# Kernel tuning notes

Measured on AMD Instinct MI355X. Metric: run time of the kernel, lower is better.

The kernel has to match this reference:

```python
import jax, jax.numpy as jnp
import numpy as np

SEQ_LEN = 252; WIN = 96; LEADS = 12; SECONDS = 10
LAYERS = 12; HEADS = 8; E = 128; FF = 512; B = 128
S = SEQ_LEN + LEADS  # 264 tokens after cls_token concat


def setup_inputs() -> dict:
    key = jax.random.key(0)
    ks = jax.random.split(key, 16)
    def n(k, shape, s=0.02):
        return jax.random.normal(k, shape, jnp.float32) * s
    return {
        "x": jax.random.normal(ks[0], (B, SEQ_LEN, WIN), jnp.float32),
        "t_indices": jax.random.randint(ks[1], (B, SEQ_LEN), 0, SECONDS + 1),
        "spatial_indices": jax.random.randint(ks[2], (B, SEQ_LEN), 0, LEADS + 1),
        "conv_w": n(ks[3], (E, WIN)),          # Conv1d k=1 == linear over window dim
        "conv_b": n(ks[4], (E,)),
        "pos_embed": n(ks[5], (1, S, E)),
        "time_tab": n(ks[6], (SECONDS + 1, E)),  # stacked time_embed_set
        "spat_tab": n(ks[7], (LEADS + 1, E)),    # stacked sqatial_embed_set
        "cls_token": n(ks[8], (1, LEADS, E)),
        "Wqkv": n(ks[9], (LAYERS, 3 * E, E)), "bqkv": jnp.zeros((LAYERS, 3 * E)),
        "Wo": n(ks[10], (LAYERS, E, E)), "bo": jnp.zeros((LAYERS, E)),
        "W1": n(ks[11], (LAYERS, FF, E)), "b1": jnp.zeros((LAYERS, FF)),
        "W2": n(ks[12], (LAYERS, E, FF)), "b2": jnp.zeros((LAYERS, E)),
        "ln1_g": jnp.ones((LAYERS, E)), "ln1_b": jnp.zeros((LAYERS, E)),
        "ln2_g": jnp.ones((LAYERS, E)), "ln2_b": jnp.zeros((LAYERS, E)),
    }


def _ln(x, g, b, eps=1e-5):
    m = x.mean(-1, keepdims=True)
    v = ((x - m) ** 2).mean(-1, keepdims=True)
    return (x - m) * jax.lax.rsqrt(v + eps) * g + b


def reference(x, t_indices, spatial_indices, conv_w, conv_b, pos_embed,
              time_tab, spat_tab, cls_token, Wqkv, bqkv, Wo, bo,
              W1, b1, W2, b2, ln1_g, ln1_b, ln2_g, ln2_b):
    Bn = x.shape[0]
    D = E // HEADS
    # kernel-size-1 Conv1d over window channels == per-token linear
    h = jnp.einsum('blt,et->ble', x, conv_w) + conv_b        # [B, L, E]
    h = jnp.concatenate([jnp.broadcast_to(cls_token, (Bn, LEADS, E)), h], axis=1)
    h = h + pos_embed                                        # [B, S, E]
    # vectorized replacement of the B*L python-loop gather
    h = h.at[:, LEADS:, :].add(time_tab[t_indices] + spat_tab[spatial_indices])
    # dropout: eval mode (identity)
    for i in range(LAYERS):  # post-norm TransformerEncoderLayer, relu FFN
        qkv = h @ Wqkv[i].T + bqkv[i]
        q, k, v = jnp.split(qkv, 3, axis=-1)
        q = q.reshape(Bn, S, HEADS, D)
        k = k.reshape(Bn, S, HEADS, D)
        v = v.reshape(Bn, S, HEADS, D)
        att = jax.nn.softmax(jnp.einsum('bqhd,bkhd->bhqk', q, k) / np.sqrt(D).astype(np.float32), axis=-1)
        o = jnp.einsum('bhqk,bkhd->bqhd', att, v).reshape(Bn, S, E) @ Wo[i].T + bo[i]
        h = _ln(h + o, ln1_g[i], ln1_b[i])
        ff = jax.nn.relu(h @ W1[i].T + b1[i]) @ W2[i].T + b2[i]
        h = _ln(h + ff, ln2_g[i], ln2_b[i])
    return h
```

## Files before the change

kernel.cpp:

```cpp
#include <hip/hip_runtime.h>

typedef unsigned short u16;
typedef __attribute__((ext_vector_type(8))) short s16x8;
typedef __attribute__((ext_vector_type(4))) float f32x4;

__device__ __forceinline__ float bf2f(u16 u) {
    union { unsigned i; float f; } v; v.i = (unsigned)u << 16; return v.f;
}
__device__ __forceinline__ u16 f2bf(float f) {
    union { float f; unsigned i; } v; v.f = f;
    unsigned r = v.i + 0x7fffu + ((v.i >> 16) & 1u);
    return (u16)(r >> 16);
}
__device__ __forceinline__ f32x4 mfma16(s16x8 a, s16x8 b, f32x4 c) {
    return __builtin_amdgcn_mfma_f32_16x16x32_bf16(a, b, c, 0, 0, 0);
}

__global__ __launch_bounds__(256)
void cvt_kernel(const float* __restrict__ src, u16* __restrict__ dst, int n)
{
    for (int i = blockIdx.x * 256 + threadIdx.x; i < n; i += gridDim.x * 256)
        dst[i] = f2bf(src[i]);
}

__global__ __launch_bounds__(256)
void embed_cls_kernel(const float* __restrict__ cls, const float* __restrict__ pos,
                      float* __restrict__ h32, u16* __restrict__ h16)
{
    int i = blockIdx.x * 256 + threadIdx.x;
    int e = i & 127, s = (i >> 7) % 12, b = i / (12 * 128);
    float v = cls[s * 128 + e] + pos[s * 128 + e];
    size_t o = ((size_t)b * 264 + s) * 128 + e;
    h32[o] = v; h16[o] = f2bf(v);
}

__global__ __launch_bounds__(256)
void embed_mfma(const u16* __restrict__ x16, const u16* __restrict__ cw16,
                const float* __restrict__ cb, const float* __restrict__ pos,
                const float* __restrict__ ttab, const float* __restrict__ stab,
                const int* __restrict__ tidx, const int* __restrict__ sidx,
                float* __restrict__ h32, u16* __restrict__ h16)
{
    const int t = threadIdx.x;
    const int wave = t >> 6, lane = t & 63;
    const int quad = lane >> 4, l16 = lane & 15;
    const int n0 = wave * 32;

    s16x8 wf[2][3];
    float bv[2];
    #pragma unroll
    for (int nt = 0; nt < 2; ++nt) {
        bv[nt] = cb[n0 + nt * 16 + l16];
        #pragma unroll
        for (int ks = 0; ks < 3; ++ks)
            wf[nt][ks] = *(const s16x8*)&cw16[(n0 + nt * 16 + l16) * 96 + ks * 32 + quad * 8];
    }
    #pragma unroll
    for (int tt = 0; tt < 4; ++tt) {
        const int m0 = (blockIdx.x * 4 + tt) * 16;
        s16x8 af[3];
        #pragma unroll
        for (int ks = 0; ks < 3; ++ks)
            af[ks] = *(const s16x8*)&x16[(size_t)(m0 + l16) * 96 + ks * 32 + quad * 8];
        f32x4 a0 = (f32x4){0.f,0.f,0.f,0.f}, a1 = (f32x4){0.f,0.f,0.f,0.f};
        #pragma unroll
        for (int ks = 0; ks < 3; ++ks) {
            a0 = mfma16(af[ks], wf[0][ks], a0);
            a1 = mfma16(af[ks], wf[1][ks], a1);
        }
        #pragma unroll
        for (int r = 0; r < 4; ++r) {
            int row = m0 + quad * 4 + r;
            int b = row / 252, l = row - b * 252;
            int ti = tidx[row], si = sidx[row];
            size_t tok = (size_t)b * 264 + 12 + l;
            #pragma unroll
            for (int nt = 0; nt < 2; ++nt) {
                int col = n0 + nt * 16 + l16;
                float v = (nt ? a1[r] : a0[r]) + bv[nt]
                        + pos[(12 + l) * 128 + col]
                        + ttab[ti * 128 + col] + stab[si * 128 + col];
                h32[tok * 128 + col] = v;
                h16[tok * 128 + col] = f2bf(v);
            }
        }
    }
}

template<bool RELU>
__global__ __launch_bounds__(256)
void gemm_bias(const u16* __restrict__ A, const u16* __restrict__ W,
               const float* __restrict__ bias, u16* __restrict__ C,
               int N, int K)
{
    const int LDK = 136;
    __shared__ alignas(16) u16 As[64 * 136];
    __shared__ alignas(16) u16 Ws[64 * 136];
    const int m0 = blockIdx.x * 64;
    const int n0 = blockIdx.y * 64;
    const int t = threadIdx.x;
    const int wave = t >> 6, lane = t & 63;
    const int quad = lane >> 4, l16 = lane & 15;
    const int wm = (wave & 1) * 32, wn = (wave >> 1) * 32;

    f32x4 acc[2][2];
    #pragma unroll
    for (int i = 0; i < 2; ++i)
        #pragma unroll
        for (int j = 0; j < 2; ++j) acc[i][j] = (f32x4){0.f, 0.f, 0.f, 0.f};

    for (int kc = 0; kc < K; kc += 128) {
        __syncthreads();
        #pragma unroll
        for (int i = 0; i < 4; ++i) {
            int id = i * 256 + t;
            int row = id >> 4, c8 = (id & 15) << 3;
            *(uint4*)&As[row * LDK + c8] = *(const uint4*)&A[(size_t)(m0 + row) * K + kc + c8];
            *(uint4*)&Ws[row * LDK + c8] = *(const uint4*)&W[(size_t)(n0 + row) * K + kc + c8];
        }
        __syncthreads();
        #pragma unroll
        for (int ks = 0; ks < 4; ++ks) {
            s16x8 a0 = *(const s16x8*)&As[(wm + l16) * LDK + ks * 32 + quad * 8];
            s16x8 a1 = *(const s16x8*)&As[(wm + 16 + l16) * LDK + ks * 32 + quad * 8];
            s16x8 b0 = *(const s16x8*)&Ws[(wn + l16) * LDK + ks * 32 + quad * 8];
            s16x8 b1 = *(const s16x8*)&Ws[(wn + 16 + l16) * LDK + ks * 32 + quad * 8];
            acc[0][0] = mfma16(a0, b0, acc[0][0]);
            acc[0][1] = mfma16(a0, b1, acc[0][1]);
            acc[1][0] = mfma16(a1, b0, acc[1][0]);
            acc[1][1] = mfma16(a1, b1, acc[1][1]);
        }
    }
    #pragma unroll
    for (int ni = 0; ni < 2; ++ni) {
        int col = n0 + wn + ni * 16 + l16;
        float bv = bias[col];
        #pragma unroll
        for (int mi = 0; mi < 2; ++mi) {
            #pragma unroll
            for (int r = 0; r < 4; ++r) {
                int row = m0 + wm + mi * 16 + quad * 4 + r;
                float v = acc[mi][ni][r] + bv;
                if (RELU) v = fmaxf(v, 0.f);
                C[(size_t)row * N + col] = f2bf(v);
            }
        }
    }
}

template<int K>
__global__ __launch_bounds__(256)
void gemm_ln(const u16* __restrict__ A, const u16* __restrict__ W,
             const float* __restrict__ bias, const float* resid,
             const float* __restrict__ g, const float* __restrict__ be,
             float* o32, u16* o16)
{
    const int LDK = 136;
    __shared__ alignas(16) u16 As[64 * 136];
    __shared__ alignas(16) u16 Ws[128 * 136];
    const int m0 = blockIdx.x * 64;
    const int t = threadIdx.x;
    const int wave = t >> 6, lane = t & 63;
    const int quad = lane >> 4, l16 = lane & 15;
    const int wr = wave * 16;

    f32x4 acc[8];
    #pragma unroll
    for (int i = 0; i < 8; ++i) acc[i] = (f32x4){0.f, 0.f, 0.f, 0.f};

    for (int kc = 0; kc < K; kc += 128) {
        __syncthreads();
        #pragma unroll
        for (int i = 0; i < 4; ++i) {
            int id = i * 256 + t;
            int row = id >> 4, c8 = (id & 15) << 3;
            *(uint4*)&As[row * LDK + c8] = *(const uint4*)&A[(size_t)(m0 + row) * K + kc + c8];
        }
        #pragma unroll
        for (int i = 0; i < 8; ++i) {
            int id = i * 256 + t;
            int row = id >> 4, c8 = (id & 15) << 3;
            *(uint4*)&Ws[row * LDK + c8] = *(const uint4*)&W[(size_t)row * K + kc + c8];
        }
        __syncthreads();
        #pragma unroll
        for (int ks = 0; ks < 4; ++ks) {
            s16x8 a = *(const s16x8*)&As[(wr + l16) * LDK + ks * 32 + quad * 8];
            #pragma unroll
            for (int nt = 0; nt < 8; ++nt) {
                s16x8 b = *(const s16x8*)&Ws[(nt * 16 + l16) * LDK + ks * 32 + quad * 8];
                acc[nt] = mfma16(a, b, acc[nt]);
            }
        }
    }
    #pragma unroll
    for (int nt = 0; nt < 8; ++nt) {
        int col = nt * 16 + l16;
        float bv = bias[col];
        #pragma unroll
        for (int r = 0; r < 4; ++r) {
            int row = m0 + wr + quad * 4 + r;
            acc[nt][r] += bv + resid[(size_t)row * 128 + col];
        }
    }
    float sm[4], sq[4];
    #pragma unroll
    for (int r = 0; r < 4; ++r) {
        float s = 0.f, q = 0.f;
        #pragma unroll
        for (int nt = 0; nt < 8; ++nt) { float v = acc[nt][r]; s += v; q += v * v; }
        sm[r] = s; sq[r] = q;
    }
    #pragma unroll
    for (int mk = 1; mk < 16; mk <<= 1) {
        #pragma unroll
        for (int r = 0; r < 4; ++r) {
            sm[r] += __shfl_xor(sm[r], mk, 64);
            sq[r] += __shfl_xor(sq[r], mk, 64);
        }
    }
    #pragma unroll
    for (int r = 0; r < 4; ++r) {
        float mean = sm[r] * (1.f / 128.f);
        float var = sq[r] * (1.f / 128.f) - mean * mean;
        float rstd = rsqrtf(var + 1e-5f);
        int row = m0 + wr + quad * 4 + r;
        #pragma unroll
        for (int nt = 0; nt < 8; ++nt) {
            int col = nt * 16 + l16;
            float y = (acc[nt][r] - mean) * rstd * g[col] + be[col];
            o32[(size_t)row * 128 + col] = y;
            o16[(size_t)row * 128 + col] = f2bf(y);
        }
    }
}

__global__ __launch_bounds__(256)
void attn_kernel(const u16* __restrict__ qkv, u16* __restrict__ ctx)
{
    const int STR = 296;
    const int KLD = 24;
    __shared__ alignas(16) u16 VT[16 * STR];
    __shared__ alignas(16) u16 Ks[272 * KLD];
    const int b = blockIdx.x >> 3, h = blockIdx.x & 7;
    const size_t base = (size_t)b * 264 * 384;
    const int t = threadIdx.x;
    const int wave = t >> 6, lane = t & 63;
    const int quad = lane >> 4, l16 = lane & 15;
    const int hq = h * 16;

    for (int i = t; i < 264 * 2; i += 256) {
        int key = i >> 1, dq = (i & 1) * 8;
        *(uint4*)&Ks[key * KLD + dq] =
            *(const uint4*)&qkv[base + (size_t)key * 384 + 128 + hq + dq];
    }
    for (int i = t; i < 264 * 16; i += 256) {
        int s = i >> 4, d = i & 15;
        VT[d * STR + s] = qkv[base + (size_t)s * 384 + 256 + hq + d];
    }
    for (int i = t; i < 16 * 32; i += 256) {
        int d = i >> 5, c = 264 + (i & 31);
        VT[d * STR + c] = 0;
    }
    __syncthreads();

    for (int qt = wave; qt < 17; qt += 4) {
        const int q0 = qt * 16;
        s16x8 qf = (s16x8){0, 0, 0, 0, 0, 0, 0, 0};
        {
            int qrow = q0 + l16;
            if (quad < 2 && qrow < 264)
                qf = *(const s16x8*)&qkv[base + (size_t)qrow * 384 + hq + quad * 8];
        }
        f32x4 sc[17];
        #pragma unroll
        for (int kt = 0; kt < 17; ++kt) {
            s16x8 kf = (s16x8){0, 0, 0, 0, 0, 0, 0, 0};
            if (quad < 2)
                kf = *(const s16x8*)&Ks[(kt * 16 + l16) * KLD + quad * 8];
            f32x4 z = (f32x4){0.f, 0.f, 0.f, 0.f};
            sc[kt] = mfma16(kf, qf, z);
        }
        float mx = -1e30f;
        #pragma unroll
        for (int kt = 0; kt < 17; ++kt) {
            #pragma unroll
            for (int r = 0; r < 4; ++r) {
                float s = sc[kt][r] * 0.25f;
                if (kt == 16 && quad >= 2) s = -1e30f;
                sc[kt][r] = s;
                mx = fmaxf(mx, s);
            }
        }
        mx = fmaxf(mx, __shfl_xor(mx, 16, 64));
        mx = fmaxf(mx, __shfl_xor(mx, 32, 64));
        float ls = 0.f;
        #pragma unroll
        for (int kt = 0; kt < 17; ++kt) {
            #pragma unroll
            for (int r = 0; r < 4; ++r) {
                float e = __expf(sc[kt][r] - mx);
                sc[kt][r] = e;
                ls += e;
            }
        }
        ls += __shfl_xor(ls, 16, 64);
        ls += __shfl_xor(ls, 32, 64);
        float rinv = 1.f / ls;

        f32x4 oa = (f32x4){0.f, 0.f, 0.f, 0.f};
        #pragma unroll
        for (int c = 0; c < 9; ++c) {
            const int kt0 = 2 * c, kt1 = 2 * c + 1;
            union { s16x8 v; u16 u[8]; } pk;
            #pragma unroll
            for (int j = 0; j < 4; ++j) pk.u[j] = f2bf(sc[kt0][j] * rinv);
            #pragma unroll
            for (int j = 0; j < 4; ++j)
                pk.u[4 + j] = (c == 8) ? (u16)0 : f2bf(sc[kt1][j] * rinv);
            union { s16x8 v; uint2 h2[2]; } vt;
            vt.h2[0] = *(const uint2*)&VT[l16 * STR + kt0 * 16 + quad * 4];
            vt.h2[1] = *(const uint2*)&VT[l16 * STR + kt1 * 16 + quad * 4];
            oa = mfma16(pk.v, vt.v, oa);
        }
        #pragma unroll
        for (int r = 0; r < 4; ++r) {
            int row = q0 + quad * 4 + r;
            if (row < 264)
                ctx[((size_t)b * 264 + row) * 128 + hq + l16] = f2bf(oa[r]);
        }
    }
}

extern "C" void kernel_launch(void* const* d_in, const int* in_sizes, int n_in,
                              void* d_out, int out_size, void* d_ws, size_t ws_size,
                              hipStream_t stream)
{
    (void)in_sizes; (void)n_in; (void)out_size; (void)ws_size;
    const float* x    = (const float*)d_in[0];
    const int*   tidx = (const int*)d_in[1];
    const int*   sidx = (const int*)d_in[2];
    const float* cw   = (const float*)d_in[3];
    const float* cb   = (const float*)d_in[4];
    const float* pos  = (const float*)d_in[5];
    const float* ttab = (const float*)d_in[6];
    const float* stab = (const float*)d_in[7];
    const float* cls  = (const float*)d_in[8];
    const float* Wqkv = (const float*)d_in[9];
    const float* bqkv = (const float*)d_in[10];
    const float* Wo   = (const float*)d_in[11];
    const float* bo   = (const float*)d_in[12];
    const float* W1   = (const float*)d_in[13];
    const float* b1   = (const float*)d_in[14];
    const float* W2   = (const float*)d_in[15];
    const float* b2   = (const float*)d_in[16];
    const float* g1   = (const float*)d_in[17];
    const float* be1  = (const float*)d_in[18];
    const float* g2   = (const float*)d_in[19];
    const float* be2  = (const float*)d_in[20];

    char* ws = (char*)d_ws;
    float* h32 = (float*)ws;
    u16* h16    = (u16*)(ws + 17301504);
    u16* big    = (u16*)(ws + 25952256);
    u16* ctx    = (u16*)(ws + 51904512);
    u16* wqkv16 = (u16*)(ws + 60555264);
    u16* wo16   = (u16*)(ws + 61734912);
    u16* w116   = (u16*)(ws + 62128128);
    u16* w216   = (u16*)(ws + 63700992);
    u16* x16    = big;
    u16* cw16   = ctx;

    cvt_kernel<<<512, 256, 0, stream>>>(Wqkv, wqkv16, 12 * 384 * 128);
    cvt_kernel<<<256, 256, 0, stream>>>(Wo,   wo16,   12 * 128 * 128);
    cvt_kernel<<<512, 256, 0, stream>>>(W1,   w116,   12 * 512 * 128);
    cvt_kernel<<<512, 256, 0, stream>>>(W2,   w216,   12 * 128 * 512);
    cvt_kernel<<<1024, 256, 0, stream>>>(x,   x16,    128 * 252 * 96);
    cvt_kernel<<<48, 256, 0, stream>>>(cw,    cw16,   128 * 96);
    embed_cls_kernel<<<768, 256, 0, stream>>>(cls, pos, h32, h16);
    embed_mfma<<<504, 256, 0, stream>>>(x16, cw16, cb, pos, ttab, stab, tidx, sidx, h32, h16);

    for (int l = 0; l < 12; ++l) {
        gemm_bias<false><<<dim3(528, 6), 256, 0, stream>>>(
            h16, wqkv16 + l * 384 * 128, bqkv + l * 384, big, 384, 128);
        attn_kernel<<<1024, 256, 0, stream>>>(big, ctx);
        gemm_ln<128><<<528, 256, 0, stream>>>(
            ctx, wo16 + l * 128 * 128, bo + l * 128, h32, g1 + l * 128, be1 + l * 128, h32, h16);
        gemm_bias<true><<<dim3(528, 8), 256, 0, stream>>>(
            h16, w116 + l * 512 * 128, b1 + l * 512, big, 512, 128);
        float* o32 = (l == 11) ? (float*)d_out : h32;
        gemm_ln<512><<<528, 256, 0, stream>>>(
            big, w216 + l * 128 * 512, b2 + l * 128, h32, g2 + l * 128, be2 + l * 128, o32, h16);
    }
}
```

Measured before the change: 1.360 ms.

## Enlarge GEMM tiles to 128x128 with XOR swizzle and streamline attention softmax

The bias GEMMs now use 128x128 block tiles with 4x4 MFMA fragments per wave and a single K=128 load, and the LN GEMMs use 128-row tiles. Both replace padded shared-memory strides with an XOR swizzle. The Q scale (1/sqrt(D)·log2e) is folded into the QKV GEMM epilogue so attention can use exp2 directly. Softmax normalization is deferred to the output, and probabilities are packed to bf16 by truncation via perm. The larger tiles halve the grid size and raise register and LDS use per block, and the truncating conversion changes rounding slightly.

```diff
diff --git a/kernel.cpp b/kernel.cpp
--- a/kernel.cpp
+++ b/kernel.cpp
@@ -11,6 +11,9 @@
     union { float f; unsigned i; } v; v.f = f;
     unsigned r = v.i + 0x7fffu + ((v.i >> 16) & 1u);
     return (u16)(r >> 16);
+}
+__device__ __forceinline__ unsigned fbits(float f) {
+    union { float f; unsigned i; } v; v.f = f; return v.i;
 }
 __device__ __forceinline__ f32x4 mfma16(s16x8 a, s16x8 b, f32x4 c) {
     return __builtin_amdgcn_mfma_f32_16x16x32_bf16(a, b, c, 0, 0, 0);
@@ -87,61 +90,62 @@
     }
 }
 
-template<bool RELU>
+template<bool RELU, bool QSCALE>
 __global__ __launch_bounds__(256)
 void gemm_bias(const u16* __restrict__ A, const u16* __restrict__ W,
-               const float* __restrict__ bias, u16* __restrict__ C,
-               int N, int K)
-{
-    const int LDK = 136;
-    __shared__ alignas(16) u16 As[64 * 136];
-    __shared__ alignas(16) u16 Ws[64 * 136];
-    const int m0 = blockIdx.x * 64;
-    const int n0 = blockIdx.y * 64;
+               const float* __restrict__ bias, u16* __restrict__ C, int N)
+{
+    __shared__ alignas(16) u16 As[128 * 128];
+    __shared__ alignas(16) u16 Ws[128 * 128];
+    const int m0 = blockIdx.x * 128;
+    const int n0 = blockIdx.y * 128;
     const int t = threadIdx.x;
     const int wave = t >> 6, lane = t & 63;
     const int quad = lane >> 4, l16 = lane & 15;
-    const int wm = (wave & 1) * 32, wn = (wave >> 1) * 32;
-
-    f32x4 acc[2][2];
-    #pragma unroll
-    for (int i = 0; i < 2; ++i)
-        #pragma unroll
-        for (int j = 0; j < 2; ++j) acc[i][j] = (f32x4){0.f, 0.f, 0.f, 0.f};
-
-    for (int kc = 0; kc < K; kc += 128) {
-        __syncthreads();
+    const int wm = (wave & 1) * 64, wn = (wave >> 1) * 64;
+
+    #pragma unroll
+    for (int i = 0; i < 8; ++i) {
+        int id = i * 256 + t;
+        int row = id >> 4, c = id & 15, sw = c ^ (row & 15);
+        *(uint4*)&As[row * 128 + sw * 8] = *(const uint4*)&A[(size_t)(m0 + row) * 128 + c * 8];
+        *(uint4*)&Ws[row * 128 + sw * 8] = *(const uint4*)&W[(size_t)(n0 + row) * 128 + c * 8];
+    }
+    __syncthreads();
+
+    f32x4 acc[4][4];
+    #pragma unroll
+    for (int i = 0; i < 4; ++i)
+        #pragma unroll
+        for (int j = 0; j < 4; ++j) acc[i][j] = (f32x4){0.f, 0.f, 0.f, 0.f};
+
+    #pragma unroll
+    for (int ks = 0; ks < 4; ++ks) {
+        const int sw = (ks * 4 + quad) ^ l16;
+        s16x8 af[4], bf[4];
         #pragma unroll
         for (int i = 0; i < 4; ++i) {
-            int id = i * 256 + t;
-            int row = id >> 4, c8 = (id & 15) << 3;
-            *(uint4*)&As[row * LDK + c8] = *(const uint4*)&A[(size_t)(m0 + row) * K + kc + c8];
-            *(uint4*)&Ws[row * LDK + c8] = *(const uint4*)&W[(size_t)(n0 + row) * K + kc + c8];
-        }
-        __syncthreads();
-        #pragma unroll
-        for (int ks = 0; ks < 4; ++ks) {
-            s16x8 a0 = *(const s16x8*)&As[(wm + l16) * LDK + ks * 32 + quad * 8];
-            s16x8 a1 = *(const s16x8*)&As[(wm + 16 + l16) * LDK + ks * 32 + quad * 8];
-            s16x8 b0 = *(const s16x8*)&Ws[(wn + l16) * LDK + ks * 32 + quad * 8];
-            s16x8 b1 = *(const s16x8*)&Ws[(wn + 16 + l16) * LDK + ks * 32 + quad * 8];
-            acc[0][0] = mfma16(a0, b0, acc[0][0]);
-            acc[0][1] = mfma16(a0, b1, acc[0][1]);
-            acc[1][0] = mfma16(a1, b0, acc[1][0]);
-            acc[1][1] = mfma16(a1, b1, acc[1][1]);
-        }
-    }
-    #pragma unroll
-    for (int ni = 0; ni < 2; ++ni) {
+            af[i] = *(const s16x8*)&As[(wm + i * 16 + l16) * 128 + sw * 8];
+            bf[i] = *(const s16x8*)&Ws[(wn + i * 16 + l16) * 128 + sw * 8];
+        }
+        #pragma unroll
+        for (int mi = 0; mi < 4; ++mi)
+            #pragma unroll
+            for (int ni = 0; ni < 4; ++ni)
+                acc[mi][ni] = mfma16(af[mi], bf[ni], acc[mi][ni]);
+    }
+    #pragma unroll
+    for (int ni = 0; ni < 4; ++ni) {
         int col = n0 + wn + ni * 16 + l16;
         float bv = bias[col];
         #pragma unroll
-        for (int mi = 0; mi < 2; ++mi) {
+        for (int mi = 0; mi < 4; ++mi) {
             #pragma unroll
             for (int r = 0; r < 4; ++r) {
                 int row = m0 + wm + mi * 16 + quad * 4 + r;
                 float v = acc[mi][ni][r] + bv;
                 if (RELU) v = fmaxf(v, 0.f);
+                if (QSCALE && blockIdx.y == 0) v *= 0.360673760222241f;
                 C[(size_t)row * N + col] = f2bf(v);
             }
         }
@@ -155,82 +159,83 @@
              const float* __restrict__ g, const float* __restrict__ be,
              float* o32, u16* o16)
 {
-    const int LDK = 136;
-    __shared__ alignas(16) u16 As[64 * 136];
-    __shared__ alignas(16) u16 Ws[128 * 136];
-    const int m0 = blockIdx.x * 64;
+    __shared__ alignas(16) u16 As[128 * 128];
+    __shared__ alignas(16) u16 Ws[128 * 128];
+    const int m0 = blockIdx.x * 128;
     const int t = threadIdx.x;
     const int wave = t >> 6, lane = t & 63;
     const int quad = lane >> 4, l16 = lane & 15;
-    const int wr = wave * 16;
-
-    f32x4 acc[8];
-    #pragma unroll
-    for (int i = 0; i < 8; ++i) acc[i] = (f32x4){0.f, 0.f, 0.f, 0.f};
+
+    f32x4 acc[2][8];
+    #pragma unroll
+    for (int i = 0; i < 2; ++i)
+        #pragma unroll
+        for (int j = 0; j < 8; ++j) acc[i][j] = (f32x4){0.f, 0.f, 0.f, 0.f};
 
     for (int kc = 0; kc < K; kc += 128) {
         __syncthreads();
         #pragma unroll
-        for (int i = 0; i < 4; ++i) {
-            int id = i * 256 + t;
-            int row = id >> 4, c8 = (id & 15) << 3;
-            *(uint4*)&As[row * LDK + c8] = *(const uint4*)&A[(size_t)(m0 + row) * K + kc + c8];
-        }
-        #pragma unroll
         for (int i = 0; i < 8; ++i) {
             int id = i * 256 + t;
-            int row = id >> 4, c8 = (id & 15) << 3;
-            *(uint4*)&Ws[row * LDK + c8] = *(const uint4*)&W[(size_t)row * K + kc + c8];
+            int row = id >> 4, c = id & 15, sw = c ^ (row & 15);
+            *(uint4*)&As[row * 128 + sw * 8] = *(const uint4*)&A[(size_t)(m0 + row) * K + kc + c * 8];
+            *(uint4*)&Ws[row * 128 + sw * 8] = *(const uint4*)&W[(size_t)row * K + kc + c * 8];
         }
         __syncthreads();
         #pragma unroll
         for (int ks = 0; ks < 4; ++ks) {
-            s16x8 a = *(const s16x8*)&As[(wr + l16) * LDK + ks * 32 + quad * 8];
+            const int sw = (ks * 4 + quad) ^ l16;
+            s16x8 a0 = *(const s16x8*)&As[(wave * 32 + l16) * 128 + sw * 8];
+            s16x8 a1 = *(const s16x8*)&As[(wave * 32 + 16 + l16) * 128 + sw * 8];
             #pragma unroll
             for (int nt = 0; nt < 8; ++nt) {
-                s16x8 b = *(const s16x8*)&Ws[(nt * 16 + l16) * LDK + ks * 32 + quad * 8];
-                acc[nt] = mfma16(a, b, acc[nt]);
-            }
-        }
-    }
-    #pragma unroll
-    for (int nt = 0; nt < 8; ++nt) {
-        int col = nt * 16 + l16;
-        float bv = bias[col];
-        #pragma unroll
-        for (int r = 0; r < 4; ++r) {
-            int row = m0 + wr + quad * 4 + r;
-            acc[nt][r] += bv + resid[(size_t)row * 128 + col];
-        }
-    }
-    float sm[4], sq[4];
-    #pragma unroll
-    for (int r = 0; r < 4; ++r) {
-        float s = 0.f, q = 0.f;
-        #pragma unroll
-        for (int nt = 0; nt < 8; ++nt) { float v = acc[nt][r]; s += v; q += v * v; }
-        sm[r] = s; sq[r] = q;
-    }
-    #pragma unroll
-    for (int mk = 1; mk < 16; mk <<= 1) {
-        #pragma unroll
-        for (int r = 0; r < 4; ++r) {
-            sm[r] += __shfl_xor(sm[r], mk, 64);
-            sq[r] += __shfl_xor(sq[r], mk, 64);
-        }
-    }
-    #pragma unroll
-    for (int r = 0; r < 4; ++r) {
-        float mean = sm[r] * (1.f / 128.f);
-        float var = sq[r] * (1.f / 128.f) - mean * mean;
-        float rstd = rsqrtf(var + 1e-5f);
-        int row = m0 + wr + quad * 4 + r;
+                s16x8 b = *(const s16x8*)&Ws[(nt * 16 + l16) * 128 + sw * 8];
+                acc[0][nt] = mfma16(a0, b, acc[0][nt]);
+                acc[1][nt] = mfma16(a1, b, acc[1][nt]);
+            }
+        }
+    }
+    #pragma unroll
+    for (int mi = 0; mi < 2; ++mi) {
         #pragma unroll
         for (int nt = 0; nt < 8; ++nt) {
             int col = nt * 16 + l16;
-            float y = (acc[nt][r] - mean) * rstd * g[col] + be[col];
-            o32[(size_t)row * 128 + col] = y;
-            o16[(size_t)row * 128 + col] = f2bf(y);
+            float bv = bias[col];
+            #pragma unroll
+            for (int r = 0; r < 4; ++r) {
+                int row = m0 + wave * 32 + mi * 16 + quad * 4 + r;
+                acc[mi][nt][r] += bv + resid[(size_t)row * 128 + col];
+            }
+        }
+        float sm[4], sq[4];
+        #pragma unroll
+        for (int r = 0; r < 4; ++r) {
+            float s = 0.f, q = 0.f;
+            #pragma unroll
+            for (int nt = 0; nt < 8; ++nt) { float v = acc[mi][nt][r]; s += v; q += v * v; }
+            sm[r] = s; sq[r] = q;
+        }
+        #pragma unroll
+        for (int mk = 1; mk < 16; mk <<= 1) {
+            #pragma unroll
+            for (int r = 0; r < 4; ++r) {
+                sm[r] += __shfl_xor(sm[r], mk, 64);
+                sq[r] += __shfl_xor(sq[r], mk, 64);
+            }
+        }
+        #pragma unroll
+        for (int r = 0; r < 4; ++r) {
+            float mean = sm[r] * (1.f / 128.f);
+            float var = sq[r] * (1.f / 128.f) - mean * mean;
+            float rstd = rsqrtf(var + 1e-5f);
+            int row = m0 + wave * 32 + mi * 16 + quad * 4 + r;
+            #pragma unroll
+            for (int nt = 0; nt < 8; ++nt) {
+                int col = nt * 16 + l16;
+                float y = (acc[mi][nt][r] - mean) * rstd * g[col] + be[col];
+                o32[(size_t)row * 128 + col] = y;
+                o16[(size_t)row * 128 + col] = f2bf(y);
+            }
         }
     }
 }
@@ -286,7 +291,7 @@
         for (int kt = 0; kt < 17; ++kt) {
             #pragma unroll
             for (int r = 0; r < 4; ++r) {
-                float s = sc[kt][r] * 0.25f;
+                float s = sc[kt][r];
                 if (kt == 16 && quad >= 2) s = -1e30f;
                 sc[kt][r] = s;
                 mx = fmaxf(mx, s);
@@ -299,7 +304,7 @@
         for (int kt = 0; kt < 17; ++kt) {
             #pragma unroll
             for (int r = 0; r < 4; ++r) {
-                float e = __expf(sc[kt][r] - mx);
+                float e = __builtin_amdgcn_exp2f(sc[kt][r] - mx);
                 sc[kt][r] = e;
                 ls += e;
             }
@@ -307,17 +312,22 @@
         ls += __shfl_xor(ls, 16, 64);
         ls += __shfl_xor(ls, 32, 64);
         float rinv = 1.f / ls;
+        float rinvT[4];
+        #pragma unroll
+        for (int r = 0; r < 4; ++r) rinvT[r] = __shfl(rinv, quad * 4 + r, 64);
 
         f32x4 oa = (f32x4){0.f, 0.f, 0.f, 0.f};
         #pragma unroll
         for (int c = 0; c < 9; ++c) {
             const int kt0 = 2 * c, kt1 = 2 * c + 1;
-            union { s16x8 v; u16 u[8]; } pk;
-            #pragma unroll
-            for (int j = 0; j < 4; ++j) pk.u[j] = f2bf(sc[kt0][j] * rinv);
-            #pragma unroll
-            for (int j = 0; j < 4; ++j)
-                pk.u[4 + j] = (c == 8) ? (u16)0 : f2bf(sc[kt1][j] * rinv);
+            union { s16x8 v; uint4 w; } pk;
+            pk.w.x = __builtin_amdgcn_perm(fbits(sc[kt0][1]), fbits(sc[kt0][0]), 0x07060302u);
+            pk.w.y = __builtin_amdgcn_perm(fbits(sc[kt0][3]), fbits(sc[kt0][2]), 0x07060302u);
+            if (c == 8) { pk.w.z = 0; pk.w.w = 0; }
+            else {
+                pk.w.z = __builtin_amdgcn_perm(fbits(sc[kt1][1]), fbits(sc[kt1][0]), 0x07060302u);
+                pk.w.w = __builtin_amdgcn_perm(fbits(sc[kt1][3]), fbits(sc[kt1][2]), 0x07060302u);
+            }
             union { s16x8 v; uint2 h2[2]; } vt;
             vt.h2[0] = *(const uint2*)&VT[l16 * STR + kt0 * 16 + quad * 4];
             vt.h2[1] = *(const uint2*)&VT[l16 * STR + kt1 * 16 + quad * 4];
@@ -327,7 +337,7 @@
         for (int r = 0; r < 4; ++r) {
             int row = q0 + quad * 4 + r;
             if (row < 264)
-                ctx[((size_t)b * 264 + row) * 128 + hq + l16] = f2bf(oa[r]);
+                ctx[((size_t)b * 264 + row) * 128 + hq + l16] = f2bf(oa[r] * rinvT[r]);
         }
     }
 }
@@ -381,15 +391,15 @@
     embed_mfma<<<504, 256, 0, stream>>>(x16, cw16, cb, pos, ttab, stab, tidx, sidx, h32, h16);
 
     for (int l = 0; l < 12; ++l) {
-        gemm_bias<false><<<dim3(528, 6), 256, 0, stream>>>(
-            h16, wqkv16 + l * 384 * 128, bqkv + l * 384, big, 384, 128);
+        gemm_bias<false, true><<<dim3(264, 3), 256, 0, stream>>>(
+            h16, wqkv16 + l * 384 * 128, bqkv + l * 384, big, 384);
         attn_kernel<<<1024, 256, 0, stream>>>(big, ctx);
-        gemm_ln<128><<<528, 256, 0, stream>>>(
+        gemm_ln<128><<<264, 256, 0, stream>>>(
             ctx, wo16 + l * 128 * 128, bo + l * 128, h32, g1 + l * 128, be1 + l * 128, h32, h16);
-        gemm_bias<true><<<dim3(528, 8), 256, 0, stream>>>(
-            h16, w116 + l * 512 * 128, b1 + l * 512, big, 512, 128);
+        gemm_bias<true, false><<<dim3(264, 4), 256, 0, stream>>>(
+            h16, w116 + l * 512 * 128, b1 + l * 512, big, 512);
         float* o32 = (l == 11) ? (float*)d_out : h32;
-        gemm_ln<512><<<528, 256, 0, stream>>>(
+        gemm_ln<512><<<264, 256, 0, stream>>>(
             big, w216 + l * 128 * 512, b2 + l * 128, h32, g2 + l * 128, be2 + l * 128, o32, h16);
     }
 }
```

New measurement: 1.434 ms. +5.4%, slower.
